# Kernel optimization log

Measured on AMD Instinct MI355X. Metric: run time of the kernel, lower is better.

## Reference

```python
import jax, jax.numpy as jnp
import numpy as np

N, E, G = 50000, 500000, 64
DIN, ED, H1, H2, HD, OUT = 128, 32, 256, 128, 64, 8


def setup_inputs() -> dict:
    key = jax.random.key(0)
    ks = jax.random.split(key, 20)
    g = lambda i, shape: (jax.random.normal(ks[i], shape, jnp.float32) * 0.05)
    return dict(
        node_attr=jax.random.normal(ks[0], (N, DIN), jnp.float32),
        edge_attr=jax.random.normal(ks[1], (E, ED), jnp.float32),
        edge_src=jax.random.randint(ks[2], (E,), 0, N, jnp.int32),
        edge_dst=jax.random.randint(ks[3], (E,), 0, N, jnp.int32),
        batch=jnp.sort(jax.random.randint(ks[4], (N,), 0, G, jnp.int32)),
        Wl1=g(5, (DIN, H1)), bl1=jnp.zeros((H1,), jnp.float32),
        Wr1=g(6, (DIN, H1)), br1=jnp.zeros((H1,), jnp.float32),
        We1=g(7, (ED, H1)), att1=g(8, (H1,)), b1=jnp.zeros((H1,), jnp.float32),
        Wl2=g(9, (H1, H2)), bl2=jnp.zeros((H2,), jnp.float32),
        Wr2=g(10, (H1, H2)), br2=jnp.zeros((H2,), jnp.float32),
        We2=g(11, (ED, H2)), att2=g(12, (H2,)), b2=jnp.zeros((H2,), jnp.float32),
        Wd1=g(13, (H2, HD)), bd1=jnp.zeros((HD,), jnp.float32),
        bn_gamma=jnp.ones((HD,), jnp.float32), bn_beta=jnp.zeros((HD,), jnp.float32),
        bn_mean=jnp.zeros((HD,), jnp.float32), bn_var=jnp.ones((HD,), jnp.float32),
        Wd2=g(14, (HD, OUT)), bd2=jnp.zeros((OUT,), jnp.float32),
    )


def gatv2(x, src, dst, eattr, Wl, bl, Wr, br, We, att, bias, n):
    # PyG GATv2Conv, heads=1: add self-loops (fill_value='mean' for edge_attr)
    ones = jnp.ones((eattr.shape[0],), x.dtype)
    deg = jax.ops.segment_sum(ones, dst, n)
    loop_attr = jax.ops.segment_sum(eattr, dst, n) / jnp.maximum(deg, 1.0)[:, None]
    loop = jnp.arange(n, dtype=src.dtype)
    src_ = jnp.concatenate([src, loop])
    dst_ = jnp.concatenate([dst, loop])
    eattr_ = jnp.concatenate([eattr, loop_attr], axis=0)
    xl = x @ Wl + bl  # [n, C] source transform (lin_l)
    xr = x @ Wr + br  # [n, C] dest transform (lin_r)
    # edge-wise GATv2 score: a^T LeakyReLU(xl_j + xr_i + We e_ij)
    e = jax.nn.leaky_relu(xl[src_] + xr[dst_] + eattr_ @ We, 0.2) @ att  # [E+n]
    m = jax.ops.segment_max(e, dst_, n)
    w = jnp.exp(e - m[dst_])
    denom = jax.ops.segment_sum(w, dst_, n)
    alpha = w / denom[dst_]
    return jax.ops.segment_sum(alpha[:, None] * xl[src_], dst_, n) + bias


def reference(node_attr, edge_attr, edge_src, edge_dst, batch,
              Wl1, bl1, Wr1, br1, We1, att1, b1,
              Wl2, bl2, Wr2, br2, We2, att2, b2,
              Wd1, bd1, bn_gamma, bn_beta, bn_mean, bn_var, Wd2, bd2):
    x = jax.nn.relu(gatv2(node_attr, edge_src, edge_dst, edge_attr,
                          Wl1, bl1, Wr1, br1, We1, att1, b1, N))
    x = jax.nn.relu(gatv2(x, edge_src, edge_dst, edge_attr,
                          Wl2, bl2, Wr2, br2, We2, att2, b2, N))
    # global mean pool over graphs
    cnt = jax.ops.segment_sum(jnp.ones((N,), x.dtype), batch, G)
    x = jax.ops.segment_sum(x, batch, G) / jnp.maximum(cnt, 1.0)[:, None]
    x = x @ Wd1 + bd1
    # BatchNorm1d in eval mode (running stats); dropout is identity in eval
    x = (x - bn_mean) / jnp.sqrt(bn_var + 1e-5) * bn_gamma + bn_beta
    x = jax.nn.leaky_relu(x, 0.1)
    return x @ Wd2 + bd2
```

## Files before the change

kernel.cpp:

```cpp
#include <hip/hip_runtime.h>
#include <cstdint>
#include <cstddef>

constexpr int Nn = 50000;
constexpr int Ne = 500000;
constexpr int Gg = 64;
constexpr int DIN = 128, ED = 32, H1 = 256, H2 = 128, HD = 64, NOUT = 8;

__global__ void count_deg_kernel(const int* __restrict__ dst, int* __restrict__ deg) {
    int e = blockIdx.x * 256 + threadIdx.x;
    if (e < Ne) atomicAdd(&deg[dst[e]], 1);
}

__global__ __launch_bounds__(1024) void scan_kernel(const int* __restrict__ deg,
                                                    int* __restrict__ row_start) {
    __shared__ int part[1024];
    int t = threadIdx.x;
    const int chunk = (Nn + 1023) / 1024;
    int lo = t * chunk;
    int hi = min(lo + chunk, Nn);
    int s = 0;
    for (int i = lo; i < hi; i++) s += deg[i];
    part[t] = s;
    __syncthreads();
    for (int off = 1; off < 1024; off <<= 1) {
        int add = (t >= off) ? part[t - off] : 0;
        __syncthreads();
        part[t] += add;
        __syncthreads();
    }
    int base = (t == 0) ? 0 : part[t - 1];
    for (int i = lo; i < hi; i++) { row_start[i] = base; base += deg[i]; }
    if (t == 0) row_start[Nn] = Ne;
}

__global__ void scatter_kernel(const int* __restrict__ dst, const int* __restrict__ row_start,
                               int* __restrict__ cursor, int* __restrict__ perm) {
    int e = blockIdx.x * 256 + threadIdx.x;
    if (e < Ne) {
        int d = dst[e];
        int p = atomicAdd(&cursor[d], 1);
        perm[row_start[d] + p] = e;
    }
}

__global__ void build_sd_kernel(const int* __restrict__ perm, const int* __restrict__ src,
                                const int* __restrict__ dst,
                                int* __restrict__ srcv, int* __restrict__ dstv) {
    int j = blockIdx.x * 256 + threadIdx.x;
    if (j < Ne) {
        int e = perm[j];
        srcv[j] = src[e];
        dstv[j] = dst[e];
    }
}

__global__ void loop_attr_kernel(const int* __restrict__ row_start, const int* __restrict__ perm,
                                 const float* __restrict__ eattr, float* __restrict__ loop_attr) {
    int tid = blockIdx.x * 256 + threadIdx.x;
    if (tid >= Nn * 8) return;
    int i = tid >> 3, q = (tid & 7) << 2;
    int r0 = row_start[i], r1 = row_start[i + 1];
    float4 s = make_float4(0.f, 0.f, 0.f, 0.f);
    for (int j = r0; j < r1; j++) {
        int e = perm[j];
        float4 v = *(const float4*)(eattr + (size_t)e * ED + q);
        s.x += v.x; s.y += v.y; s.z += v.z; s.w += v.w;
    }
    float inv = 1.0f / fmaxf((float)(r1 - r0), 1.0f);
    *(float4*)(loop_attr + (size_t)i * ED + q) =
        make_float4(s.x * inv, s.y * inv, s.z * inv, s.w * inv);
}

__global__ __launch_bounds__(256) void gemm_bias2_kernel(const float* __restrict__ A,
                                                         const float* __restrict__ W0,
                                                         const float* __restrict__ bias0,
                                                         float* __restrict__ C0,
                                                         const float* __restrict__ W1,
                                                         const float* __restrict__ bias1,
                                                         float* __restrict__ C1,
                                                         int M, int K, int Ncols) {
    const float* W = blockIdx.z ? W1 : W0;
    const float* bias = blockIdx.z ? bias1 : bias0;
    float* C = blockIdx.z ? C1 : C0;
    __shared__ float As[16][68];
    __shared__ float Bs[16][68];
    const int m0 = blockIdx.y * 64, n0 = blockIdx.x * 64;
    const int tid = threadIdx.x;
    const int tx = tid & 15, ty = tid >> 4;
    float acc[4][4] = {};
    const int ar = tid >> 2, ac4 = (tid & 3) << 2;
    const int br = tid >> 4, bc4 = (tid & 15) << 2;
    for (int k0 = 0; k0 < K; k0 += 16) {
        float4 av = make_float4(0.f, 0.f, 0.f, 0.f);
        if (m0 + ar < M) av = *(const float4*)(A + (size_t)(m0 + ar) * K + k0 + ac4);
        As[ac4 + 0][ar] = av.x; As[ac4 + 1][ar] = av.y;
        As[ac4 + 2][ar] = av.z; As[ac4 + 3][ar] = av.w;
        float4 bv = *(const float4*)(W + (size_t)(k0 + br) * Ncols + n0 + bc4);
        *(float4*)&Bs[br][bc4] = bv;
        __syncthreads();
#pragma unroll
        for (int k = 0; k < 16; k++) {
            float a[4], b[4];
#pragma unroll
            for (int i = 0; i < 4; i++) a[i] = As[k][ty * 4 + i];
#pragma unroll
            for (int j = 0; j < 4; j++) b[j] = Bs[k][tx * 4 + j];
#pragma unroll
            for (int i = 0; i < 4; i++)
#pragma unroll
                for (int j = 0; j < 4; j++) acc[i][j] = fmaf(a[i], b[j], acc[i][j]);
        }
        __syncthreads();
    }
#pragma unroll
    for (int i = 0; i < 4; i++) {
        int m = m0 + ty * 4 + i;
        if (m < M) {
            float4 o;
            o.x = acc[i][0] + bias[n0 + tx * 4 + 0];
            o.y = acc[i][1] + bias[n0 + tx * 4 + 1];
            o.z = acc[i][2] + bias[n0 + tx * 4 + 2];
            o.w = acc[i][3] + bias[n0 + tx * 4 + 3];
            *(float4*)(C + (size_t)m * Ncols + n0 + tx * 4) = o;
        }
    }
}

template <int C>
__global__ __launch_bounds__(256) void score_gemm2_kernel(
    int count, const int* __restrict__ perm,
    const int* __restrict__ srcv, const int* __restrict__ dstv,
    const float* __restrict__ attr,
    const float* __restrict__ xl, const float* __restrict__ xr,
    const float* __restrict__ We, const float* __restrict__ att,
    float* __restrict__ sc_out) {
    __shared__ float As[32][68];
    __shared__ float Bs[32][68];
    const int m0 = blockIdx.x * 64;
    const int tid = threadIdx.x, tx = tid & 15, ty = tid >> 4;

    {
        int ar = tid >> 2, ac8 = (tid & 3) << 3;
        int row = min(m0 + ar, count - 1);
        int e = perm ? perm[row] : row;
        const float* s = attr + (size_t)e * ED + ac8;
        float4 v0 = *(const float4*)s;
        float4 v1 = *(const float4*)(s + 4);
        As[ac8 + 0][ar] = v0.x; As[ac8 + 1][ar] = v0.y;
        As[ac8 + 2][ar] = v0.z; As[ac8 + 3][ar] = v0.w;
        As[ac8 + 4][ar] = v1.x; As[ac8 + 5][ar] = v1.y;
        As[ac8 + 6][ar] = v1.z; As[ac8 + 7][ar] = v1.w;
    }

    int rs[4], rd[4];
#pragma unroll
    for (int i = 0; i < 4; i++) {
        int j = min(m0 + ty * 4 + i, count - 1);
        rs[i] = srcv ? srcv[j] : j;
        rd[i] = dstv ? dstv[j] : j;
    }

    float p[4] = {0.f, 0.f, 0.f, 0.f};

    for (int n0 = 0; n0 < C; n0 += 64) {
        {
            int br = tid >> 3, bc8 = (tid & 7) << 3;
            const float* s = We + (size_t)br * C + n0 + bc8;
            *(float4*)&Bs[br][bc8] = *(const float4*)s;
            *(float4*)&Bs[br][bc8 + 4] = *(const float4*)(s + 4);
        }
        __syncthreads();

        float acc[4][4] = {};
#pragma unroll
        for (int k = 0; k < ED; k++) {
            float4 av = *(const float4*)&As[k][ty * 4];
            float4 bv = *(const float4*)&Bs[k][tx * 4];
            float a[4] = {av.x, av.y, av.z, av.w};
            float b[4] = {bv.x, bv.y, bv.z, bv.w};
#pragma unroll
            for (int i = 0; i < 4; i++)
#pragma unroll
                for (int j = 0; j < 4; j++) acc[i][j] = fmaf(a[i], b[j], acc[i][j]);
        }

        float attv[4];
#pragma unroll
        for (int j = 0; j < 4; j++) attv[j] = att[n0 + tx * 4 + j];
#pragma unroll
        for (int i = 0; i < 4; i++) {
            float4 a4 = *(const float4*)(xl + (size_t)rs[i] * C + n0 + tx * 4);
            float4 b4 = *(const float4*)(xr + (size_t)rd[i] * C + n0 + tx * 4);
            float xs4[4] = {a4.x + b4.x, a4.y + b4.y, a4.z + b4.z, a4.w + b4.w};
#pragma unroll
            for (int j = 0; j < 4; j++) {
                float v = acc[i][j] + xs4[j];
                v = v > 0.f ? v : 0.2f * v;
                p[i] = fmaf(v, attv[j], p[i]);
            }
        }
        __syncthreads();
    }

#pragma unroll
    for (int i = 0; i < 4; i++) {
        float q = p[i];
        q += __shfl_xor(q, 1);
        q += __shfl_xor(q, 2);
        q += __shfl_xor(q, 4);
        q += __shfl_xor(q, 8);
        int r = m0 + ty * 4 + i;
        if (tx == 0 && r < count) sc_out[r] = q;
    }
}

template <int C>
__global__ __launch_bounds__(256) void aggregate2_kernel(
    const int* __restrict__ row_start, const int* __restrict__ srcv,
    const float* __restrict__ scores, const float* __restrict__ sscore,
    const float* __restrict__ xl, const float* __restrict__ bias,
    float* __restrict__ xout) {
    constexpr int VP = C / 64;
    const int wave = threadIdx.x >> 6, lane = threadIdx.x & 63;
    const int i = blockIdx.x * 4 + wave;
    if (i >= Nn) return;
    const int r0 = row_start[i], r1 = row_start[i + 1];

    float mx = sscore[i];
    for (int j = r0 + lane; j < r1; j += 64) mx = fmaxf(mx, scores[j]);
#pragma unroll
    for (int off = 32; off >= 1; off >>= 1) mx = fmaxf(mx, __shfl_xor(mx, off));

    float l = 0.f;
    float acc[VP];
#pragma unroll
    for (int j = 0; j < VP; j++) acc[j] = 0.f;

    for (int j0 = r0; j0 < r1; j0 += 4) {
        const int nb = min(4, r1 - j0);
        float w4[4], xs[4][VP];
#pragma unroll
        for (int q = 0; q < 4; q++) {
            int j = min(j0 + q, r1 - 1);
            w4[q] = scores[j];
            const float* p = xl + (size_t)srcv[j] * C + lane * VP;
            if constexpr (VP == 4) {
                float4 v = *(const float4*)p;
                xs[q][0] = v.x; xs[q][1] = v.y; xs[q][2] = v.z; xs[q][3] = v.w;
            } else {
                float2 v = *(const float2*)p;
                xs[q][0] = v.x; xs[q][1] = v.y;
            }
        }
        for (int q = 0; q < nb; q++) {
            float w = __expf(w4[q] - mx);
            l += w;
#pragma unroll
            for (int j = 0; j < VP; j++) acc[j] = fmaf(w, xs[q][j], acc[j]);
        }
    }

    {
        float w = __expf(sscore[i] - mx);
        l += w;
        const float* p = xl + (size_t)i * C + lane * VP;
        if constexpr (VP == 4) {
            float4 v = *(const float4*)p;
            acc[0] = fmaf(w, v.x, acc[0]); acc[1] = fmaf(w, v.y, acc[1]);
            acc[2] = fmaf(w, v.z, acc[2]); acc[3] = fmaf(w, v.w, acc[3]);
        } else {
            float2 v = *(const float2*)p;
            acc[0] = fmaf(w, v.x, acc[0]); acc[1] = fmaf(w, v.y, acc[1]);
        }
    }

    float invl = 1.0f / l;
    float* xo = xout + (size_t)i * C + lane * VP;
    if constexpr (VP == 4) {
        float4 bv = *(const float4*)(bias + lane * 4);
        float4 o;
        o.x = fmaxf(fmaf(acc[0], invl, bv.x), 0.f);
        o.y = fmaxf(fmaf(acc[1], invl, bv.y), 0.f);
        o.z = fmaxf(fmaf(acc[2], invl, bv.z), 0.f);
        o.w = fmaxf(fmaf(acc[3], invl, bv.w), 0.f);
        *(float4*)xo = o;
    } else {
        float2 bv = *(const float2*)(bias + lane * 2);
        float2 o;
        o.x = fmaxf(fmaf(acc[0], invl, bv.x), 0.f);
        o.y = fmaxf(fmaf(acc[1], invl, bv.y), 0.f);
        *(float2*)xo = o;
    }
}

__global__ __launch_bounds__(128) void pool2_kernel(const float* __restrict__ x2,
                                                    const int* __restrict__ batch,
                                                    float* __restrict__ pooled,
                                                    float* __restrict__ cnt) {
    const int c = threadIdx.x;
    const int chunk = (Nn + gridDim.x - 1) / gridDim.x;
    int lo = blockIdx.x * chunk;
    int hi = min(lo + chunk, Nn);
    if (lo >= hi) return;
    int gcur = batch[lo];
    float acc = 0.f, ncnt = 0.f;
    for (int i = lo; i < hi; i++) {
        int g = batch[i];
        if (g != gcur) {
            atomicAdd(&pooled[gcur * H2 + c], acc);
            if (c == 0) atomicAdd(&cnt[gcur], ncnt);
            acc = 0.f; ncnt = 0.f; gcur = g;
        }
        acc += x2[(size_t)i * H2 + c];
        ncnt += 1.f;
    }
    atomicAdd(&pooled[gcur * H2 + c], acc);
    if (c == 0) atomicAdd(&cnt[gcur], ncnt);
}

__global__ __launch_bounds__(64) void head_kernel(
    const float* __restrict__ pooled, const float* __restrict__ cnt,
    const float* __restrict__ Wd1, const float* __restrict__ bd1,
    const float* __restrict__ gamma, const float* __restrict__ beta,
    const float* __restrict__ mean, const float* __restrict__ var,
    const float* __restrict__ Wd2, const float* __restrict__ bd2,
    float* __restrict__ out) {
    __shared__ float xm[H2];
    __shared__ float h[HD];
    int g = blockIdx.x, t = threadIdx.x;
    float c = fmaxf(cnt[g], 1.0f);
    for (int i = t; i < H2; i += 64) xm[i] = pooled[g * H2 + i] / c;
    __syncthreads();
    float a = bd1[t];
    for (int k = 0; k < H2; k++) a = fmaf(xm[k], Wd1[k * HD + t], a);
    a = (a - mean[t]) / sqrtf(var[t] + 1e-5f) * gamma[t] + beta[t];
    a = a > 0.f ? a : 0.1f * a;
    h[t] = a;
    __syncthreads();
    if (t < NOUT) {
        float o = bd2[t];
        for (int k = 0; k < HD; k++) o = fmaf(h[k], Wd2[k * NOUT + t], o);
        out[g * NOUT + t] = o;
    }
}

extern "C" void kernel_launch(void* const* d_in, const int* in_sizes, int n_in,
                              void* d_out, int out_size, void* d_ws, size_t ws_size,
                              hipStream_t stream) {
    const float* node_attr = (const float*)d_in[0];
    const float* edge_attr = (const float*)d_in[1];
    const int* edge_src = (const int*)d_in[2];
    const int* edge_dst = (const int*)d_in[3];
    const int* batch = (const int*)d_in[4];
    const float* Wl1 = (const float*)d_in[5];  const float* bl1 = (const float*)d_in[6];
    const float* Wr1 = (const float*)d_in[7];  const float* br1 = (const float*)d_in[8];
    const float* We1 = (const float*)d_in[9];  const float* att1 = (const float*)d_in[10];
    const float* b1 = (const float*)d_in[11];
    const float* Wl2 = (const float*)d_in[12]; const float* bl2 = (const float*)d_in[13];
    const float* Wr2 = (const float*)d_in[14]; const float* br2 = (const float*)d_in[15];
    const float* We2 = (const float*)d_in[16]; const float* att2 = (const float*)d_in[17];
    const float* b2 = (const float*)d_in[18];
    const float* Wd1 = (const float*)d_in[19]; const float* bd1 = (const float*)d_in[20];
    const float* bn_gamma = (const float*)d_in[21]; const float* bn_beta = (const float*)d_in[22];
    const float* bn_mean = (const float*)d_in[23];  const float* bn_var = (const float*)d_in[24];
    const float* Wd2 = (const float*)d_in[25]; const float* bd2 = (const float*)d_in[26];
    float* out = (float*)d_out;

    char* ws = (char*)d_ws;
    size_t off = 0;
    auto alloc = [&](size_t bytes) -> char* {
        char* p = ws + off;
        off = (off + bytes + 255) & ~(size_t)255;
        return p;
    };
    int* deg         = (int*)alloc((size_t)Nn * 4);
    int* row_start   = (int*)alloc((size_t)(Nn + 1) * 4);
    int* cursor      = (int*)alloc((size_t)Nn * 4);
    int* perm        = (int*)alloc((size_t)Ne * 4);
    int* srcv        = (int*)alloc((size_t)Ne * 4);
    int* dstv        = (int*)alloc((size_t)Ne * 4);
    float* loop_attr = (float*)alloc((size_t)Nn * ED * 4);
    float* scores    = (float*)alloc((size_t)Ne * 4);
    float* sscore    = (float*)alloc((size_t)Nn * 4);
    float* pooled    = (float*)alloc((size_t)Gg * H2 * 4);
    float* cnt       = (float*)alloc((size_t)Gg * 4);
    float* xlb       = (float*)alloc((size_t)Nn * H1 * 4);
    float* xrb       = (float*)alloc((size_t)Nn * H1 * 4);
    float* x1        = (float*)alloc((size_t)Nn * H1 * 4);

    hipMemsetAsync(deg, 0, (size_t)Nn * 4, stream);
    hipMemsetAsync(cursor, 0, (size_t)Nn * 4, stream);
    hipMemsetAsync(pooled, 0, (size_t)Gg * H2 * 4, stream);
    hipMemsetAsync(cnt, 0, (size_t)Gg * 4, stream);

    count_deg_kernel<<<(Ne + 255) / 256, 256, 0, stream>>>(edge_dst, deg);
    scan_kernel<<<1, 1024, 0, stream>>>(deg, row_start);
    scatter_kernel<<<(Ne + 255) / 256, 256, 0, stream>>>(edge_dst, row_start, cursor, perm);
    build_sd_kernel<<<(Ne + 255) / 256, 256, 0, stream>>>(perm, edge_src, edge_dst, srcv, dstv);
    loop_attr_kernel<<<(Nn * 8 + 255) / 256, 256, 0, stream>>>(row_start, perm, edge_attr, loop_attr);

    const int eb = (Ne + 63) / 64, nbk = (Nn + 63) / 64;

    gemm_bias2_kernel<<<dim3(H1 / 64, (Nn + 63) / 64, 2), 256, 0, stream>>>(
        node_attr, Wl1, bl1, xlb, Wr1, br1, xrb, Nn, DIN, H1);
    score_gemm2_kernel<H1><<<eb, 256, 0, stream>>>(
        Ne, perm, srcv, dstv, edge_attr, xlb, xrb, We1, att1, scores);
    score_gemm2_kernel<H1><<<nbk, 256, 0, stream>>>(
        Nn, nullptr, nullptr, nullptr, loop_attr, xlb, xrb, We1, att1, sscore);
    aggregate2_kernel<H1><<<(Nn + 3) / 4, 256, 0, stream>>>(
        row_start, srcv, scores, sscore, xlb, b1, x1);

    gemm_bias2_kernel<<<dim3(H2 / 64, (Nn + 63) / 64, 2), 256, 0, stream>>>(
        x1, Wl2, bl2, xlb, Wr2, br2, xrb, Nn, H1, H2);
    score_gemm2_kernel<H2><<<eb, 256, 0, stream>>>(
        Ne, perm, srcv, dstv, edge_attr, xlb, xrb, We2, att2, scores);
    score_gemm2_kernel<H2><<<nbk, 256, 0, stream>>>(
        Nn, nullptr, nullptr, nullptr, loop_attr, xlb, xrb, We2, att2, sscore);
    float* x2 = x1;
    aggregate2_kernel<H2><<<(Nn + 3) / 4, 256, 0, stream>>>(
        row_start, srcv, scores, sscore, xlb, b2, x2);

    pool2_kernel<<<256, 128, 0, stream>>>(x2, batch, pooled, cnt);
    head_kernel<<<Gg, 64, 0, stream>>>(pooled, cnt, Wd1, bd1, bn_gamma, bn_beta,
                                       bn_mean, bn_var, Wd2, bd2, out);
}
```

Baseline: 946.9 us.

## Software-prefetch next tiles in GEMM, score, and aggregate kernels

Adds register double-buffering in three kernels. The dense GEMM loads the next K-slice of A and W into registers while computing on the current shared-memory tile. The edge score kernel prefetches the next 64-column chunk of gathered xl/xr rows during the small We GEMM, and the aggregation kernel loads the next batch of four neighbour rows before processing the current one. The aim is to hide global and gather latency behind compute, at the cost of extra registers that may reduce occupancy.

```diff
diff --git a/kernel.cpp b/kernel.cpp
--- a/kernel.cpp
+++ b/kernel.cpp
@@ -91,14 +91,21 @@
     float acc[4][4] = {};
     const int ar = tid >> 2, ac4 = (tid & 3) << 2;
     const int br = tid >> 4, bc4 = (tid & 15) << 2;
+    const bool arow_ok = (m0 + ar < M);
+
+    float4 av = make_float4(0.f, 0.f, 0.f, 0.f);
+    if (arow_ok) av = *(const float4*)(A + (size_t)(m0 + ar) * K + ac4);
+    float4 bv = *(const float4*)(W + (size_t)br * Ncols + n0 + bc4);
+
     for (int k0 = 0; k0 < K; k0 += 16) {
-        float4 av = make_float4(0.f, 0.f, 0.f, 0.f);
-        if (m0 + ar < M) av = *(const float4*)(A + (size_t)(m0 + ar) * K + k0 + ac4);
         As[ac4 + 0][ar] = av.x; As[ac4 + 1][ar] = av.y;
         As[ac4 + 2][ar] = av.z; As[ac4 + 3][ar] = av.w;
-        float4 bv = *(const float4*)(W + (size_t)(k0 + br) * Ncols + n0 + bc4);
         *(float4*)&Bs[br][bc4] = bv;
         __syncthreads();
+        if (k0 + 16 < K) {
+            if (arow_ok) av = *(const float4*)(A + (size_t)(m0 + ar) * K + k0 + 16 + ac4);
+            bv = *(const float4*)(W + (size_t)(k0 + 16 + br) * Ncols + n0 + bc4);
+        }
 #pragma unroll
         for (int k = 0; k < 16; k++) {
             float a[4], b[4];
@@ -128,7 +135,7 @@
 }
 
 template <int C>
-__global__ __launch_bounds__(256) void score_gemm2_kernel(
+__global__ __launch_bounds__(256) void score_gemm3_kernel(
     int count, const int* __restrict__ perm,
     const int* __restrict__ srcv, const int* __restrict__ dstv,
     const float* __restrict__ attr,
@@ -161,6 +168,13 @@
         rd[i] = dstv ? dstv[j] : j;
     }
 
+    float4 ga[4], gb[4];
+#pragma unroll
+    for (int i = 0; i < 4; i++) {
+        ga[i] = *(const float4*)(xl + (size_t)rs[i] * C + tx * 4);
+        gb[i] = *(const float4*)(xr + (size_t)rd[i] * C + tx * 4);
+    }
+
     float p[4] = {0.f, 0.f, 0.f, 0.f};
 
     for (int n0 = 0; n0 < C; n0 += 64) {
@@ -172,6 +186,15 @@
         }
         __syncthreads();
 
+        float4 na[4], nb[4];
+        if (n0 + 64 < C) {
+#pragma unroll
+            for (int i = 0; i < 4; i++) {
+                na[i] = *(const float4*)(xl + (size_t)rs[i] * C + n0 + 64 + tx * 4);
+                nb[i] = *(const float4*)(xr + (size_t)rd[i] * C + n0 + 64 + tx * 4);
+            }
+        }
+
         float acc[4][4] = {};
 #pragma unroll
         for (int k = 0; k < ED; k++) {
@@ -190,9 +213,8 @@
         for (int j = 0; j < 4; j++) attv[j] = att[n0 + tx * 4 + j];
 #pragma unroll
         for (int i = 0; i < 4; i++) {
-            float4 a4 = *(const float4*)(xl + (size_t)rs[i] * C + n0 + tx * 4);
-            float4 b4 = *(const float4*)(xr + (size_t)rd[i] * C + n0 + tx * 4);
-            float xs4[4] = {a4.x + b4.x, a4.y + b4.y, a4.z + b4.z, a4.w + b4.w};
+            float xs4[4] = {ga[i].x + gb[i].x, ga[i].y + gb[i].y,
+                            ga[i].z + gb[i].z, ga[i].w + gb[i].w};
 #pragma unroll
             for (int j = 0; j < 4; j++) {
                 float v = acc[i][j] + xs4[j];
@@ -201,6 +223,10 @@
             }
         }
         __syncthreads();
+        if (n0 + 64 < C) {
+#pragma unroll
+            for (int i = 0; i < 4; i++) { ga[i] = na[i]; gb[i] = nb[i]; }
+        }
     }
 
 #pragma unroll
@@ -237,27 +263,41 @@
 #pragma unroll
     for (int j = 0; j < VP; j++) acc[j] = 0.f;
 
-    for (int j0 = r0; j0 < r1; j0 += 4) {
-        const int nb = min(4, r1 - j0);
-        float w4[4], xs[4][VP];
+    float wA[4], xA[4][VP];
+    auto load_batch = [&](int j0, float* w, float (*x)[VP]) {
 #pragma unroll
         for (int q = 0; q < 4; q++) {
             int j = min(j0 + q, r1 - 1);
-            w4[q] = scores[j];
+            w[q] = scores[j];
             const float* p = xl + (size_t)srcv[j] * C + lane * VP;
             if constexpr (VP == 4) {
                 float4 v = *(const float4*)p;
-                xs[q][0] = v.x; xs[q][1] = v.y; xs[q][2] = v.z; xs[q][3] = v.w;
+                x[q][0] = v.x; x[q][1] = v.y; x[q][2] = v.z; x[q][3] = v.w;
             } else {
                 float2 v = *(const float2*)p;
-                xs[q][0] = v.x; xs[q][1] = v.y;
+                x[q][0] = v.x; x[q][1] = v.y;
             }
         }
+    };
+    if (r0 < r1) load_batch(r0, wA, xA);
+
+    for (int j0 = r0; j0 < r1; j0 += 4) {
+        float wB[4], xB[4][VP];
+        if (j0 + 4 < r1) load_batch(j0 + 4, wB, xB);
+        const int nb = min(4, r1 - j0);
         for (int q = 0; q < nb; q++) {
-            float w = __expf(w4[q] - mx);
+            float w = __expf(wA[q] - mx);
             l += w;
 #pragma unroll
-            for (int j = 0; j < VP; j++) acc[j] = fmaf(w, xs[q][j], acc[j]);
+            for (int j = 0; j < VP; j++) acc[j] = fmaf(w, xA[q][j], acc[j]);
+        }
+        if (j0 + 4 < r1) {
+#pragma unroll
+            for (int q = 0; q < 4; q++) {
+                wA[q] = wB[q];
+#pragma unroll
+                for (int j = 0; j < VP; j++) xA[q][j] = xB[q][j];
+            }
         }
     }
 
@@ -404,18 +444,18 @@
 
     gemm_bias2_kernel<<<dim3(H1 / 64, (Nn + 63) / 64, 2), 256, 0, stream>>>(
         node_attr, Wl1, bl1, xlb, Wr1, br1, xrb, Nn, DIN, H1);
-    score_gemm2_kernel<H1><<<eb, 256, 0, stream>>>(
+    score_gemm3_kernel<H1><<<eb, 256, 0, stream>>>(
         Ne, perm, srcv, dstv, edge_attr, xlb, xrb, We1, att1, scores);
-    score_gemm2_kernel<H1><<<nbk, 256, 0, stream>>>(
+    score_gemm3_kernel<H1><<<nbk, 256, 0, stream>>>(
         Nn, nullptr, nullptr, nullptr, loop_attr, xlb, xrb, We1, att1, sscore);
     aggregate2_kernel<H1><<<(Nn + 3) / 4, 256, 0, stream>>>(
         row_start, srcv, scores, sscore, xlb, b1, x1);
 
     gemm_bias2_kernel<<<dim3(H2 / 64, (Nn + 63) / 64, 2), 256, 0, stream>>>(
         x1, Wl2, bl2, xlb, Wr2, br2, xrb, Nn, H1, H2);
-    score_gemm2_kernel<H2><<<eb, 256, 0, stream>>>(
+    score_gemm3_kernel<H2><<<eb, 256, 0, stream>>>(
         Ne, perm, srcv, dstv, edge_attr, xlb, xrb, We2, att2, scores);
-    score_gemm2_kernel<H2><<<nbk, 256, 0, stream>>>(
+    score_gemm3_kernel<H2><<<nbk, 256, 0, stream>>>(
         Nn, nullptr, nullptr, nullptr, loop_attr, xlb, xrb, We2, att2, sscore);
     float* x2 = x1;
     aggregate2_kernel<H2><<<(Nn + 3) / 4, 256, 0, stream>>>(
```

Result: slower. 966.5 us (+2.1%).
